# Optimization experiments

Hardware: AMD Instinct MI355X
Metric: run time of the kernel (lower is better)

The kernel has to match this reference:

```python
import jax, jax.numpy as jnp
import numpy as np

MIN_C = 1e-5   # base_c * DYNAMIC_CURVATURE_MIN_RATIO
MAX_C = 10.0   # base_c * DYNAMIC_CURVATURE_MAX_RATIO
T = 0.7
EPS = 1e-7
B, IN_DIM, HID, OUT_DIM = 4096, 4096, 4096, 1024


def _artanh(x):
    x = jnp.clip(x, -1.0 + 1e-5, 1.0 - 1e-5)
    return 0.5 * jnp.log1p(2.0 * x / (1.0 - x))


def _mobius_scalar_mul(r, x, c):
    # r: python float, x: [B,D], c: [B,1] per-row curvature
    sqrt_c = jnp.sqrt(c)
    norm = jnp.clip(jnp.linalg.norm(x, axis=-1, keepdims=True), EPS)
    arg = jnp.clip(sqrt_c * norm, EPS, 1.0 - 1e-5)
    return jnp.tanh(r * _artanh(arg)) * x / (sqrt_c * norm)


def _mobius_add(x, y, c):
    xy = jnp.sum(x * y, axis=-1, keepdims=True)
    x2 = jnp.sum(x * x, axis=-1, keepdims=True)
    y2 = jnp.sum(y * y, axis=-1, keepdims=True)
    num = (1.0 + 2.0 * c * xy + c * y2) * x + (1.0 - c * x2) * y
    den = 1.0 + 2.0 * c * xy + c * c * x2 * y2
    return num / jnp.clip(den, EPS)


def poincare_ball_layer(h, u, c, t):
    # geodesic-style layer: ((1-t) (*) h) (+) (t (*) u) on the Poincare ball
    return _mobius_add(_mobius_scalar_mul(1.0 - t, h, c),
                       _mobius_scalar_mul(t, u, c), c)


def setup_inputs() -> dict:
    key = jax.random.key(0)
    ks = jax.random.split(key, 8)
    std = 0.02  # WEIGHT_INIT_STD_IMPROVED
    return {
        "x": jax.random.normal(ks[0], (B, IN_DIM), jnp.float32),
        "W1": jax.random.normal(ks[1], (IN_DIM, HID), jnp.float32) * std,
        "b1": jnp.zeros((HID,), jnp.float32),
        "W2": jax.random.normal(ks[2], (HID, HID), jnp.float32) * std,
        "b2": jnp.zeros((HID,), jnp.float32),
        "Wout": jax.random.normal(ks[3], (HID, OUT_DIM), jnp.float32) * std,
        "bout": jnp.zeros((OUT_DIM,), jnp.float32),
        "curv_feat": jax.random.normal(ks[4], (16,), jnp.float32) * 0.01,
        "curv_scale": jnp.ones((1,), jnp.float32) * 0.1,
        "proj": jax.random.normal(ks[5], (IN_DIM, 16), jnp.float32),
    }


def reference(x, W1, b1, W2, b2, Wout, bout, curv_feat, curv_scale, proj):
    x_flat = x.reshape(x.shape[0], -1)
    h = jnp.tanh(x_flat @ W1 + b1)            # [B, HID]
    u = jax.nn.sigmoid(h @ W2 + b2)           # [B, HID]
    # adaptive curvature prediction (vectorized over batch)
    x_red = x_flat @ proj                     # [B, 16]
    feat_inter = x_red @ curv_feat            # [B]
    adj = jax.nn.sigmoid(feat_inter + curv_scale[0])
    c = MIN_C + (MAX_C - MIN_C) * adj         # [B]
    c = jnp.clip(c, MIN_C, MAX_C)[:, None]    # [B, 1]
    z = poincare_ball_layer(h, u, c, T)
    # NaN fallback per row (mirrors torch per-sample isnan check)
    z = jnp.where(jnp.any(jnp.isnan(z), axis=1, keepdims=True), h, z)
    return z @ Wout + bout
```

## Files before the change

kernel.cpp:

```cpp
#include <hip/hip_runtime.h>
#include <hip/hip_bf16.h>
#include <math.h>


typedef __attribute__((ext_vector_type(8)))  __bf16 bf16x8;
typedef __attribute__((ext_vector_type(4)))  float  f32x4;
typedef __attribute__((ext_vector_type(8)))  unsigned short us8;

constexpr int BATCH = 4096;
constexpr int IND   = 4096;
constexpr int HIDD  = 4096;
constexpr int OUTD  = 1024;
constexpr float T_C  = 0.7f;
constexpr float MINC = 1e-5f;
constexpr float MAXC = 10.0f;
constexpr float EPSV = 1e-7f;

__device__ __forceinline__ float bf2f(unsigned int us) {
    return __uint_as_float(us << 16);
}
__device__ __forceinline__ unsigned short f2bf(float f) {
    unsigned int u = __float_as_uint(f);
    u = (u + 0x7FFFu + ((u >> 16) & 1u)) >> 16;
    return (unsigned short)u;
}
__device__ __forceinline__ void stage16(const char* src, const unsigned short* dst) {
    __builtin_amdgcn_global_load_lds(
        (const __attribute__((address_space(1))) unsigned int*)src,
        (__attribute__((address_space(3))) unsigned int*)dst, 16, 0, 0);
}

__global__ __launch_bounds__(256)
void cast_curv(const float* __restrict__ x, const float* __restrict__ v,
               const float* __restrict__ cs,
               unsigned short* __restrict__ xb, float* __restrict__ c)
{
    const int row = blockIdx.x;
    const float* xr = x + (size_t)row * IND;
    unsigned short* ob = xb + (size_t)row * IND;
    float s = 0.f;
    for (int i = threadIdx.x; i < IND / 4; i += 256) {
        float4 w  = ((const float4*)xr)[i];
        float4 vv = ((const float4*)v)[i];
        s += w.x * vv.x + w.y * vv.y + w.z * vv.z + w.w * vv.w;
        ushort4 o;
        o.x = f2bf(w.x); o.y = f2bf(w.y); o.z = f2bf(w.z); o.w = f2bf(w.w);
        ((ushort4*)ob)[i] = o;
    }
    #pragma unroll
    for (int o = 32; o > 0; o >>= 1) s += __shfl_down(s, o, 64);
    __shared__ float red[4];
    if ((threadIdx.x & 63) == 0) red[threadIdx.x >> 6] = s;
    __syncthreads();
    if (threadIdx.x == 0) {
        float tot = red[0] + red[1] + red[2] + red[3];
        float adj = 1.0f / (1.0f + expf(-(tot + cs[0])));
        float cc  = MINC + (MAXC - MINC) * adj;
        c[row] = fminf(fmaxf(cc, MINC), MAXC);
    }
}

__global__ __launch_bounds__(256)
void transpose_cast64(const float* __restrict__ in, unsigned short* __restrict__ out,
                      int K, int N)
{
    __shared__ float tile[64][65];
    const int k0 = blockIdx.y * 64;
    const int n0 = blockIdx.x * 64;
    const int t = threadIdx.x;
    #pragma unroll
    for (int i = 0; i < 4; i++) {
        const int idx = i * 256 + t;
        const int r = idx >> 4, c4 = (idx & 15) * 4;
        float4 v = *(const float4*)(&in[(size_t)(k0 + r) * N + n0 + c4]);
        tile[r][c4 + 0] = v.x; tile[r][c4 + 1] = v.y;
        tile[r][c4 + 2] = v.z; tile[r][c4 + 3] = v.w;
    }
    __syncthreads();
    #pragma unroll
    for (int j = 0; j < 2; j++) {
        const int idx = j * 256 + t;
        const int r = idx >> 3, c8 = (idx & 7) * 8;
        us8 o;
        #pragma unroll
        for (int e = 0; e < 8; e++) o[e] = f2bf(tile[c8 + e][r]);
        *(us8*)(&out[(size_t)(n0 + r) * K + k0 + c8]) = o;
    }
}

template<int EPI>
__global__ __launch_bounds__(512, 2)
void gemm256(const unsigned short* __restrict__ A,
             const unsigned short* __restrict__ Bt,
             const float* __restrict__ bias,
             unsigned short* __restrict__ outp,
             int N, int K)
{
    __shared__ unsigned short lds[4 * 256 * 64];

    const int t = threadIdx.x;
    const int w = t >> 6, l = t & 63;
    const int wr = w >> 2, wc = w & 3;
    const int lr = l & 15, lg = l >> 4;

    const int nwg = gridDim.x * gridDim.y;
    const int bid = blockIdx.y * gridDim.x + blockIdx.x;
    const int q8 = nwg >> 3, r8 = nwg & 7;
    const int xcd = bid & 7, off = bid >> 3;
    const int wgid = (xcd < r8 ? xcd * (q8 + 1) : r8 * (q8 + 1) + (xcd - r8) * q8) + off;
    const int by = wgid / gridDim.x;
    const int bx = wgid % gridDim.x;

    const int row0 = by * 256, col0 = bx * 256;
    const unsigned short* Ab = A  + (size_t)row0 * K;
    const unsigned short* Bb = Bt + (size_t)col0 * K;
    const int NT = K >> 6;

    f32x4 acc[8][4] = {};

    const int id0 = t, id1 = 512 + t;
    const int r0 = id0 >> 3, r1 = id1 >> 3;
    const int cb0 = (id0 & 7) * 16, cb1 = (id1 & 7) * 16;
    const int s0 = cb0 ^ ((r0 & 7) << 4), s1 = cb1 ^ ((r1 & 7) << 4);
    const size_t K2 = (size_t)K * 2;
    const char* pA00 = (const char*)Ab + (size_t)r0 * K2 + s0;
    const char* pA01 = (const char*)Ab + (size_t)r1 * K2 + s1;
    const char* pA10 = pA00 + 128 * K2;
    const char* pA11 = pA01 + 128 * K2;
    const char* pB00 = (const char*)Bb + (size_t)r0 * K2 + s0;
    const char* pB01 = (const char*)Bb + (size_t)r1 * K2 + s1;
    const char* pB10 = pB00 + 128 * K2;
    const char* pB11 = pB01 + 128 * K2;
    const int dA0a = id0 * 8,          dA0b = id1 * 8;
    const int dA1a = 8192 + id0 * 8,   dA1b = 8192 + id1 * 8;
    const int dB0a = 32768 + id0 * 8,  dB0b = 32768 + id1 * 8;
    const int dB1a = 40960 + id0 * 8,  dB1b = 40960 + id1 * 8;

    const int sw = (lr & 7) << 4;
    const int c0 = (lg * 16) ^ sw;
    const int c1 = (64 + lg * 16) ^ sw;
    const int aofc0 = (wr * 16 + lr) * 128 + c0;
    const int aofc1 = (wr * 16 + lr) * 128 + c1;
    const int bofc0 = 65536 + (wc * 64 + lr) * 128 + c0;
    const int bofc1 = 65536 + (wc * 64 + lr) * 128 + c1;
    const char* ldsb = (const char*)lds;

    stage16(pA00, lds + dA0a); stage16(pA01, lds + dA0b);
    stage16(pB00, lds + dB0a); stage16(pB01, lds + dB0b);
    stage16(pB10, lds + dB1a); stage16(pB11, lds + dB1b);
    stage16(pA10, lds + dA1a); stage16(pA11, lds + dA1b);
    asm volatile("s_waitcnt vmcnt(0)" ::: "memory");
    __builtin_amdgcn_s_barrier();

    for (int kt = 0; kt < NT; ++kt) {
        const int buf = kt & 1, nb = buf ^ 1;
        const bool pre = (kt + 1 < NT);
        pA00 += 128; pA01 += 128; pA10 += 128; pA11 += 128;
        pB00 += 128; pB01 += 128; pB10 += 128; pB11 += 128;
        const int bufby = buf * 32768;
        const int bsh   = nb * 16384;
        const char* rA0 = ldsb + bufby + aofc0;
        const char* rA1 = ldsb + bufby + aofc1;
        const char* rB0 = ldsb + bufby + bofc0;
        const char* rB1 = ldsb + bufby + bofc1;

        if (pre) {
            stage16(pA00, lds + bsh + dA0a); stage16(pA01, lds + bsh + dA0b);
            stage16(pB00, lds + bsh + dB0a); stage16(pB01, lds + bsh + dB0b);
            stage16(pB10, lds + bsh + dB1a); stage16(pB11, lds + bsh + dB1b);
            stage16(pA10, lds + bsh + dA1a); stage16(pA11, lds + bsh + dA1b);
        }

        bf16x8 bfk[4], afk[4];

        #pragma unroll
        for (int ni = 0; ni < 4; ni++) bfk[ni] = *(const bf16x8*)(rB0 + ni * 2048);
        #pragma unroll
        for (int mi = 0; mi < 4; mi++) afk[mi] = *(const bf16x8*)(rA0 + mi * 4096);
        __builtin_amdgcn_s_setprio(1);
        #pragma unroll
        for (int mi = 0; mi < 4; mi++)
            #pragma unroll
            for (int ni = 0; ni < 4; ni++)
                acc[mi][ni] = __builtin_amdgcn_mfma_f32_16x16x32_bf16(
                    afk[mi], bfk[ni], acc[mi][ni], 0, 0, 0);
        __builtin_amdgcn_s_setprio(0);

        #pragma unroll
        for (int mi = 0; mi < 4; mi++) afk[mi] = *(const bf16x8*)(rA0 + 16384 + mi * 4096);
        __builtin_amdgcn_s_setprio(1);
        #pragma unroll
        for (int mi = 0; mi < 4; mi++)
            #pragma unroll
            for (int ni = 0; ni < 4; ni++)
                acc[4 + mi][ni] = __builtin_amdgcn_mfma_f32_16x16x32_bf16(
                    afk[mi], bfk[ni], acc[4 + mi][ni], 0, 0, 0);
        __builtin_amdgcn_s_setprio(0);

        #pragma unroll
        for (int ni = 0; ni < 4; ni++) bfk[ni] = *(const bf16x8*)(rB1 + ni * 2048);
        #pragma unroll
        for (int mi = 0; mi < 4; mi++) afk[mi] = *(const bf16x8*)(rA1 + mi * 4096);
        __builtin_amdgcn_s_setprio(1);
        #pragma unroll
        for (int mi = 0; mi < 4; mi++)
            #pragma unroll
            for (int ni = 0; ni < 4; ni++)
                acc[mi][ni] = __builtin_amdgcn_mfma_f32_16x16x32_bf16(
                    afk[mi], bfk[ni], acc[mi][ni], 0, 0, 0);
        __builtin_amdgcn_s_setprio(0);

        #pragma unroll
        for (int mi = 0; mi < 4; mi++) afk[mi] = *(const bf16x8*)(rA1 + 16384 + mi * 4096);
        __builtin_amdgcn_s_setprio(1);
        #pragma unroll
        for (int mi = 0; mi < 4; mi++)
            #pragma unroll
            for (int ni = 0; ni < 4; ni++)
                acc[4 + mi][ni] = __builtin_amdgcn_mfma_f32_16x16x32_bf16(
                    afk[mi], bfk[ni], acc[4 + mi][ni], 0, 0, 0);
        __builtin_amdgcn_s_setprio(0);

        asm volatile("s_waitcnt vmcnt(0)" ::: "memory");
        __builtin_amdgcn_s_barrier();
    }

    const int colb = col0 + wc * 64;
    #pragma unroll
    for (int ni = 0; ni < 4; ni++) {
        const int cg = colb + ni * 16 + lr;
        const float bv = bias[cg];
        #pragma unroll
        for (int mi = 0; mi < 8; mi++) {
            #pragma unroll
            for (int r = 0; r < 4; r++) {
                const int rg = row0 + wr * 16 + mi * 32 + lg * 4 + r;
                float v = acc[mi][ni][r] + bv;
                if constexpr (EPI == 0) v = tanhf(v);
                else                    v = 1.0f / (1.0f + expf(-v));
                outp[(size_t)rg * N + cg] = f2bf(v);
            }
        }
    }
}

__global__ __launch_bounds__(512, 2)
void gemm_out128(const unsigned short* __restrict__ A,
                 const unsigned short* __restrict__ Bt,
                 const float* __restrict__ bias,
                 float* __restrict__ outp,
                 int N, int K)
{
    __shared__ unsigned short lds[32768];

    const int t = threadIdx.x;
    const int w = t >> 6, l = t & 63;
    const int wr = w >> 2, wc = w & 3;
    const int lr = l & 15, lg = l >> 4;

    const int nwg = gridDim.x * gridDim.y;
    const int bid = blockIdx.y * gridDim.x + blockIdx.x;
    const int q8 = nwg >> 3, r8 = nwg & 7;
    const int xcd = bid & 7, off = bid >> 3;
    const int wgid = (xcd < r8 ? xcd * (q8 + 1) : r8 * (q8 + 1) + (xcd - r8) * q8) + off;
    const int by = wgid / gridDim.x;
    const int bx = wgid % gridDim.x;

    const int row0 = by * 128, col0 = bx * 128;
    const unsigned short* Ab = A  + (size_t)row0 * K;
    const unsigned short* Bb = Bt + (size_t)col0 * K;
    const int NT = K >> 6;

    f32x4 acc[4][2] = {};

    const int sr = t >> 2;
    const int scb = ((t & 3) * 16) ^ ((sr & 3) << 4);
    const size_t K2 = (size_t)K * 2;
    const char* pAk0 = (const char*)Ab + (size_t)sr * K2 + scb;
    const char* pAk1 = pAk0 + 64;
    const char* pBk0 = (const char*)Bb + (size_t)sr * K2 + scb;
    const char* pBk1 = pBk0 + 64;
    const int dAk0 = t * 8,          dAk1 = 4096 + t * 8;
    const int dBk0 = 16384 + t * 8,  dBk1 = 20480 + t * 8;

    const int csw = (lg * 16) ^ ((lr & 3) << 4);
    const int aof = (wr * 64 + lr) * 64 + csw;
    const int bof = 32768 + (wc * 32 + lr) * 64 + csw;
    const char* ldsb = (const char*)lds;

    stage16(pAk0, lds + dAk0); stage16(pBk0, lds + dBk0);
    stage16(pAk1, lds + dAk1); stage16(pBk1, lds + dBk1);
    asm volatile("s_waitcnt vmcnt(0)" ::: "memory");
    __builtin_amdgcn_s_barrier();

    for (int kt = 0; kt < NT; ++kt) {
        const int buf = kt & 1, nb = buf ^ 1;
        const bool pre = (kt + 1 < NT);
        pAk0 += 128; pAk1 += 128; pBk0 += 128; pBk1 += 128;
        const int bufby = buf * 16384;
        const int bsh   = nb * 8192;
        const char* rA0 = ldsb + bufby + aof;
        const char* rB0 = ldsb + bufby + bof;
        const char* rA1 = rA0 + 8192;
        const char* rB1 = rB0 + 8192;

        if (pre) {
            stage16(pAk0, lds + bsh + dAk0); stage16(pBk0, lds + bsh + dBk0);
            stage16(pAk1, lds + bsh + dAk1); stage16(pBk1, lds + bsh + dBk1);
        }

        bf16x8 af[4], bfr[2];

        #pragma unroll
        for (int nj = 0; nj < 2; nj++) bfr[nj] = *(const bf16x8*)(rB0 + nj * 1024);
        #pragma unroll
        for (int mi = 0; mi < 4; mi++) af[mi] = *(const bf16x8*)(rA0 + mi * 1024);
        __builtin_amdgcn_s_setprio(1);
        #pragma unroll
        for (int mi = 0; mi < 4; mi++)
            #pragma unroll
            for (int nj = 0; nj < 2; nj++)
                acc[mi][nj] = __builtin_amdgcn_mfma_f32_16x16x32_bf16(
                    af[mi], bfr[nj], acc[mi][nj], 0, 0, 0);
        __builtin_amdgcn_s_setprio(0);

        #pragma unroll
        for (int nj = 0; nj < 2; nj++) bfr[nj] = *(const bf16x8*)(rB1 + nj * 1024);
        #pragma unroll
        for (int mi = 0; mi < 4; mi++) af[mi] = *(const bf16x8*)(rA1 + mi * 1024);
        __builtin_amdgcn_s_setprio(1);
        #pragma unroll
        for (int mi = 0; mi < 4; mi++)
            #pragma unroll
            for (int nj = 0; nj < 2; nj++)
                acc[mi][nj] = __builtin_amdgcn_mfma_f32_16x16x32_bf16(
                    af[mi], bfr[nj], acc[mi][nj], 0, 0, 0);
        __builtin_amdgcn_s_setprio(0);

        asm volatile("s_waitcnt vmcnt(0)" ::: "memory");
        __builtin_amdgcn_s_barrier();
    }

    #pragma unroll
    for (int nj = 0; nj < 2; nj++) {
        const int cg = col0 + wc * 32 + nj * 16 + lr;
        const float bv = bias[cg];
        #pragma unroll
        for (int mi = 0; mi < 4; mi++)
            #pragma unroll
            for (int r = 0; r < 4; r++) {
                const int rg = row0 + wr * 64 + mi * 16 + lg * 4 + r;
                outp[(size_t)rg * N + cg] = acc[mi][nj][r] + bv;
            }
    }
}

__global__ __launch_bounds__(256)
void proj_cf(const float* __restrict__ proj, const float* __restrict__ cf,
             float* __restrict__ v)
{
    int i = blockIdx.x * 256 + threadIdx.x;
    if (i < IND) {
        float s = 0.f;
        #pragma unroll
        for (int j = 0; j < 16; j++) s += proj[i * 16 + j] * cf[j];
        v[i] = s;
    }
}

__global__ __launch_bounds__(256)
void poincare_kernel(const unsigned short* __restrict__ hb,
                     const unsigned short* __restrict__ ub,
                     const float* __restrict__ c,
                     unsigned short* __restrict__ zb)
{
    const int row = blockIdx.x;
    const int t = threadIdx.x;
    const size_t base = (size_t)row * HIDD;

    float hv[16], uv[16];
    float h2 = 0.f, u2 = 0.f, hu = 0.f;
    #pragma unroll
    for (int q = 0; q < 2; q++) {
        const int e0 = (q * 256 + t) * 8;
        uint4 hc = *(const uint4*)(hb + base + e0);
        uint4 uc = *(const uint4*)(ub + base + e0);
        const unsigned int hw[4] = {hc.x, hc.y, hc.z, hc.w};
        const unsigned int uw[4] = {uc.x, uc.y, uc.z, uc.w};
        #pragma unroll
        for (int i = 0; i < 4; i++) {
            float h0 = bf2f(hw[i] & 0xFFFFu), h1 = bf2f(hw[i] >> 16);
            float u0 = bf2f(uw[i] & 0xFFFFu), u1 = bf2f(uw[i] >> 16);
            hv[q * 8 + 2 * i]     = h0; hv[q * 8 + 2 * i + 1] = h1;
            uv[q * 8 + 2 * i]     = u0; uv[q * 8 + 2 * i + 1] = u1;
            h2 += h0 * h0 + h1 * h1;
            u2 += u0 * u0 + u1 * u1;
            hu += h0 * u0 + h1 * u1;
        }
    }
    #pragma unroll
    for (int o = 32; o > 0; o >>= 1) {
        h2 += __shfl_down(h2, o, 64);
        u2 += __shfl_down(u2, o, 64);
        hu += __shfl_down(hu, o, 64);
    }
    __shared__ float red[3][4];
    const int w = t >> 6;
    if ((t & 63) == 0) { red[0][w] = h2; red[1][w] = u2; red[2][w] = hu; }
    __syncthreads();
    h2 = red[0][0] + red[0][1] + red[0][2] + red[0][3];
    u2 = red[1][0] + red[1][1] + red[1][2] + red[1][3];
    hu = red[2][0] + red[2][1] + red[2][2] + red[2][3];

    const float cc = c[row];
    const float sc = sqrtf(cc);
    float nh = fmaxf(sqrtf(h2), EPSV);
    float nu = fmaxf(sqrtf(u2), EPSV);
    float ah = fminf(fmaxf(sc * nh, EPSV), 1.0f - 1e-5f);
    float au = fminf(fmaxf(sc * nu, EPSV), 1.0f - 1e-5f);
    float ath = 0.5f * log1pf(2.0f * ah / (1.0f - ah));
    float atu = 0.5f * log1pf(2.0f * au / (1.0f - au));
    float alpha = tanhf((1.0f - T_C) * ath) / (sc * nh);
    float beta  = tanhf(T_C * atu) / (sc * nu);
    float x2 = alpha * alpha * h2;
    float y2 = beta * beta * u2;
    float xy = alpha * beta * hu;
    float den = 1.0f + 2.0f * cc * xy + cc * cc * x2 * y2;
    den = fmaxf(den, EPSV);
    float ca = (1.0f + 2.0f * cc * xy + cc * y2) * alpha / den;
    float cb = (1.0f - cc * x2) * beta / den;
    if (isnan(ca) || isnan(cb)) { ca = 1.0f; cb = 0.0f; }

    #pragma unroll
    for (int q = 0; q < 2; q++) {
        const int e0 = (q * 256 + t) * 8;
        unsigned int ow[4];
        #pragma unroll
        for (int i = 0; i < 4; i++) {
            float z0 = ca * hv[q * 8 + 2 * i]     + cb * uv[q * 8 + 2 * i];
            float z1 = ca * hv[q * 8 + 2 * i + 1] + cb * uv[q * 8 + 2 * i + 1];
            ow[i] = (unsigned int)f2bf(z0) | ((unsigned int)f2bf(z1) << 16);
        }
        *(uint4*)(zb + base + e0) = make_uint4(ow[0], ow[1], ow[2], ow[3]);
    }
}

extern "C" void kernel_launch(void* const* d_in, const int* in_sizes, int n_in,
                              void* d_out, int out_size, void* d_ws, size_t ws_size,
                              hipStream_t stream)
{
    const float* x    = (const float*)d_in[0];
    const float* W1   = (const float*)d_in[1];
    const float* b1   = (const float*)d_in[2];
    const float* W2   = (const float*)d_in[3];
    const float* b2   = (const float*)d_in[4];
    const float* Wout = (const float*)d_in[5];
    const float* bout = (const float*)d_in[6];
    const float* cf   = (const float*)d_in[7];
    const float* cs   = (const float*)d_in[8];
    const float* proj = (const float*)d_in[9];
    float* out = (float*)d_out;

    char* ws = (char*)d_ws;
    unsigned short* x_bf = (unsigned short*)(ws);
    unsigned short* w_bf = (unsigned short*)(ws + (33554432));
    unsigned short* h_bf = (unsigned short*)(ws + (67108864));
    unsigned short* u_bf = (unsigned short*)(ws + (100663296));
    float* vvec = (float*)(ws + 134217728);
    float* cvec = (float*)(ws + 134217728 + 16384);

    proj_cf<<<IND / 256, 256, 0, stream>>>(proj, cf, vvec);
    cast_curv<<<BATCH, 256, 0, stream>>>(x, vvec, cs, x_bf, cvec);

    transpose_cast64<<<dim3(HIDD / 64, IND / 64), 256, 0, stream>>>(W1, w_bf, IND, HIDD);
    gemm256<0><<<dim3(HIDD / 256, BATCH / 256), 512, 0, stream>>>(x_bf, w_bf, b1, h_bf, HIDD, IND);

    transpose_cast64<<<dim3(HIDD / 64, HIDD / 64), 256, 0, stream>>>(W2, w_bf, HIDD, HIDD);
    gemm256<1><<<dim3(HIDD / 256, BATCH / 256), 512, 0, stream>>>(h_bf, w_bf, b2, u_bf, HIDD, HIDD);

    poincare_kernel<<<BATCH, 256, 0, stream>>>(h_bf, u_bf, cvec, x_bf);

    transpose_cast64<<<dim3(OUTD / 64, HIDD / 64), 256, 0, stream>>>(Wout, w_bf, HIDD, OUTD);
    gemm_out128<<<dim3(OUTD / 128, BATCH / 128), 512, 0, stream>>>(x_bf, w_bf, bout, out, OUTD, HIDD);
}
```

Baseline: 387.6 us.

## Restructure 256x256 GEMM main loop into fine-grained staged pipeline

Reorganizes the LDS layout of the 256-tile GEMM so A and B live in separate half-buffers, and B is prefetched two K-steps ahead while A is prefetched one step ahead. Each K-step is split into four phases, each interleaving small A-fragment LDS reads, one piece of global-to-LDS staging, barriers and 16 MFMAs. The goal is to spread memory traffic across the MFMA work and avoid the large end-of-iteration vmcnt(0) stall. Warp row mapping changes to contiguous 128-row halves. In exchange it adds many more barriers per iteration and depends on fragile vmcnt accounting.

```diff
diff --git a/kernel.cpp b/kernel.cpp
--- a/kernel.cpp
+++ b/kernel.cpp
@@ -96,7 +96,7 @@
              unsigned short* __restrict__ outp,
              int N, int K)
 {
-    __shared__ unsigned short lds[4 * 256 * 64];
+    __shared__ unsigned short lds[65536];
 
     const int t = threadIdx.x;
     const int w = t >> 6, l = t & 63;
@@ -120,8 +120,8 @@
 
     const int id0 = t, id1 = 512 + t;
     const int r0 = id0 >> 3, r1 = id1 >> 3;
-    const int cb0 = (id0 & 7) * 16, cb1 = (id1 & 7) * 16;
-    const int s0 = cb0 ^ ((r0 & 7) << 4), s1 = cb1 ^ ((r1 & 7) << 4);
+    const int s0 = ((id0 & 7) * 16) ^ ((r0 & 7) << 4);
+    const int s1 = ((id1 & 7) * 16) ^ ((r1 & 7) << 4);
     const size_t K2 = (size_t)K * 2;
     const char* pA00 = (const char*)Ab + (size_t)r0 * K2 + s0;
     const char* pA01 = (const char*)Ab + (size_t)r1 * K2 + s1;
@@ -133,96 +133,104 @@
     const char* pB11 = pB01 + 128 * K2;
     const int dA0a = id0 * 8,          dA0b = id1 * 8;
     const int dA1a = 8192 + id0 * 8,   dA1b = 8192 + id1 * 8;
-    const int dB0a = 32768 + id0 * 8,  dB0b = 32768 + id1 * 8;
-    const int dB1a = 40960 + id0 * 8,  dB1b = 40960 + id1 * 8;
+    const int dB0a = 16384 + id0 * 8,  dB0b = 16384 + id1 * 8;
+    const int dB1a = 24576 + id0 * 8,  dB1b = 24576 + id1 * 8;
 
     const int sw = (lr & 7) << 4;
     const int c0 = (lg * 16) ^ sw;
     const int c1 = (64 + lg * 16) ^ sw;
-    const int aofc0 = (wr * 16 + lr) * 128 + c0;
-    const int aofc1 = (wr * 16 + lr) * 128 + c1;
-    const int bofc0 = 65536 + (wc * 64 + lr) * 128 + c0;
-    const int bofc1 = 65536 + (wc * 64 + lr) * 128 + c1;
+    const int aof = (wr * 128 + lr) * 128;
+    const int bof = 32768 + (wc * 64 + lr) * 128;
     const char* ldsb = (const char*)lds;
 
     stage16(pA00, lds + dA0a); stage16(pA01, lds + dA0b);
+    stage16(pA10, lds + dA1a); stage16(pA11, lds + dA1b);
     stage16(pB00, lds + dB0a); stage16(pB01, lds + dB0b);
     stage16(pB10, lds + dB1a); stage16(pB11, lds + dB1b);
-    stage16(pA10, lds + dA1a); stage16(pA11, lds + dA1b);
-    asm volatile("s_waitcnt vmcnt(0)" ::: "memory");
+    stage16(pB00 + 128, lds + 32768 + dB0a); stage16(pB01 + 128, lds + 32768 + dB0b);
+    stage16(pB10 + 128, lds + 32768 + dB1a); stage16(pB11 + 128, lds + 32768 + dB1b);
+    asm volatile("s_waitcnt vmcnt(4)" ::: "memory");
     __builtin_amdgcn_s_barrier();
+    pB00 += 128; pB01 += 128; pB10 += 128; pB11 += 128;
 
     for (int kt = 0; kt < NT; ++kt) {
         const int buf = kt & 1, nb = buf ^ 1;
-        const bool pre = (kt + 1 < NT);
         pA00 += 128; pA01 += 128; pA10 += 128; pA11 += 128;
         pB00 += 128; pB01 += 128; pB10 += 128; pB11 += 128;
-        const int bufby = buf * 32768;
-        const int bsh   = nb * 16384;
-        const char* rA0 = ldsb + bufby + aofc0;
-        const char* rA1 = ldsb + bufby + aofc1;
-        const char* rB0 = ldsb + bufby + bofc0;
-        const char* rB1 = ldsb + bufby + bofc1;
-
-        if (pre) {
-            stage16(pA00, lds + bsh + dA0a); stage16(pA01, lds + bsh + dA0b);
-            stage16(pB00, lds + bsh + dB0a); stage16(pB01, lds + bsh + dB0b);
-            stage16(pB10, lds + bsh + dB1a); stage16(pB11, lds + bsh + dB1b);
-            stage16(pA10, lds + bsh + dA1a); stage16(pA11, lds + bsh + dA1b);
-        }
-
-        bf16x8 bfk[4], afk[4];
-
-        #pragma unroll
-        for (int ni = 0; ni < 4; ni++) bfk[ni] = *(const bf16x8*)(rB0 + ni * 2048);
-        #pragma unroll
-        for (int mi = 0; mi < 4; mi++) afk[mi] = *(const bf16x8*)(rA0 + mi * 4096);
+        const bool preA = (kt + 1 < NT);
+        const bool preB = (kt + 2 < NT);
+        const char* rA = ldsb + buf * 65536 + aof;
+        const char* rB = ldsb + buf * 65536 + bof;
+        unsigned short* sbA = lds + nb * 32768;
+        unsigned short* sbB = lds + buf * 32768;
+
+        bf16x8 bB[4][2], aF[2][2];
+
+        #pragma unroll
+        for (int ni = 0; ni < 4; ni++) {
+            bB[ni][0] = *(const bf16x8*)(rB + ni * 2048 + c0);
+            bB[ni][1] = *(const bf16x8*)(rB + ni * 2048 + c1);
+        }
+        aF[0][0] = *(const bf16x8*)(rA + 0 * 2048 + c0);
+        aF[0][1] = *(const bf16x8*)(rA + 0 * 2048 + c1);
+        aF[1][0] = *(const bf16x8*)(rA + 1 * 2048 + c0);
+        aF[1][1] = *(const bf16x8*)(rA + 1 * 2048 + c1);
+        if (preA) { stage16(pA00, sbA + dA0a); stage16(pA01, sbA + dA0b); }
+        __builtin_amdgcn_sched_barrier(0);
+        __builtin_amdgcn_s_barrier();
+        asm volatile("s_waitcnt lgkmcnt(0)" ::: "memory");
+        __builtin_amdgcn_sched_barrier(0);
         __builtin_amdgcn_s_setprio(1);
         #pragma unroll
-        for (int mi = 0; mi < 4; mi++)
+        for (int s = 0; s < 2; s++)
             #pragma unroll
             for (int ni = 0; ni < 4; ni++)
-                acc[mi][ni] = __builtin_amdgcn_mfma_f32_16x16x32_bf16(
-                    afk[mi], bfk[ni], acc[mi][ni], 0, 0, 0);
+                acc[s][ni] = __builtin_amdgcn_mfma_f32_16x16x32_bf16(
+                    aF[s][0], bB[ni][0], acc[s][ni], 0, 0, 0);
+        #pragma unroll
+        for (int s = 0; s < 2; s++)
+            #pragma unroll
+            for (int ni = 0; ni < 4; ni++)
+                acc[s][ni] = __builtin_amdgcn_mfma_f32_16x16x32_bf16(
+                    aF[s][1], bB[ni][1], acc[s][ni], 0, 0, 0);
         __builtin_amdgcn_s_setprio(0);
-
-        #pragma unroll
-        for (int mi = 0; mi < 4; mi++) afk[mi] = *(const bf16x8*)(rA0 + 16384 + mi * 4096);
-        __builtin_amdgcn_s_setprio(1);
-        #pragma unroll
-        for (int mi = 0; mi < 4; mi++)
-            #pragma unroll
-            for (int ni = 0; ni < 4; ni++)
-                acc[4 + mi][ni] = __builtin_amdgcn_mfma_f32_16x16x32_bf16(
-                    afk[mi], bfk[ni], acc[4 + mi][ni], 0, 0, 0);
-        __builtin_amdgcn_s_setprio(0);
-
-        #pragma unroll
-        for (int ni = 0; ni < 4; ni++) bfk[ni] = *(const bf16x8*)(rB1 + ni * 2048);
-        #pragma unroll
-        for (int mi = 0; mi < 4; mi++) afk[mi] = *(const bf16x8*)(rA1 + mi * 4096);
-        __builtin_amdgcn_s_setprio(1);
-        #pragma unroll
-        for (int mi = 0; mi < 4; mi++)
-            #pragma unroll
-            for (int ni = 0; ni < 4; ni++)
-                acc[mi][ni] = __builtin_amdgcn_mfma_f32_16x16x32_bf16(
-                    afk[mi], bfk[ni], acc[mi][ni], 0, 0, 0);
-        __builtin_amdgcn_s_setprio(0);
-
-        #pragma unroll
-        for (int mi = 0; mi < 4; mi++) afk[mi] = *(const bf16x8*)(rA1 + 16384 + mi * 4096);
-        __builtin_amdgcn_s_setprio(1);
-        #pragma unroll
-        for (int mi = 0; mi < 4; mi++)
-            #pragma unroll
-            for (int ni = 0; ni < 4; ni++)
-                acc[4 + mi][ni] = __builtin_amdgcn_mfma_f32_16x16x32_bf16(
-                    afk[mi], bfk[ni], acc[4 + mi][ni], 0, 0, 0);
-        __builtin_amdgcn_s_setprio(0);
-
-        asm volatile("s_waitcnt vmcnt(0)" ::: "memory");
+        __builtin_amdgcn_sched_barrier(0);
         __builtin_amdgcn_s_barrier();
+
+        #pragma unroll
+        for (int p = 1; p < 4; p++) {
+            aF[0][0] = *(const bf16x8*)(rA + (2 * p) * 2048 + c0);
+            aF[0][1] = *(const bf16x8*)(rA + (2 * p) * 2048 + c1);
+            aF[1][0] = *(const bf16x8*)(rA + (2 * p + 1) * 2048 + c0);
+            aF[1][1] = *(const bf16x8*)(rA + (2 * p + 1) * 2048 + c1);
+            if (p == 1 && preA) { stage16(pA10, sbA + dA1a); stage16(pA11, sbA + dA1b); }
+            if (p == 2 && preB) { stage16(pB00, sbB + dB0a); stage16(pB01, sbB + dB0b); }
+            if (p == 3 && preB) { stage16(pB10, sbB + dB1a); stage16(pB11, sbB + dB1b); }
+            __builtin_amdgcn_sched_barrier(0);
+            __builtin_amdgcn_s_barrier();
+            asm volatile("s_waitcnt lgkmcnt(0)" ::: "memory");
+            __builtin_amdgcn_sched_barrier(0);
+            __builtin_amdgcn_s_setprio(1);
+            #pragma unroll
+            for (int s = 0; s < 2; s++)
+                #pragma unroll
+                for (int ni = 0; ni < 4; ni++)
+                    acc[2 * p + s][ni] = __builtin_amdgcn_mfma_f32_16x16x32_bf16(
+                        aF[s][0], bB[ni][0], acc[2 * p + s][ni], 0, 0, 0);
+            #pragma unroll
+            for (int s = 0; s < 2; s++)
+                #pragma unroll
+                for (int ni = 0; ni < 4; ni++)
+                    acc[2 * p + s][ni] = __builtin_amdgcn_mfma_f32_16x16x32_bf16(
+                        aF[s][1], bB[ni][1], acc[2 * p + s][ni], 0, 0, 0);
+            __builtin_amdgcn_s_setprio(0);
+            __builtin_amdgcn_sched_barrier(0);
+            if (p == 3) {
+                if (preB) asm volatile("s_waitcnt vmcnt(4)" ::: "memory");
+                else      asm volatile("s_waitcnt vmcnt(0)" ::: "memory");
+            }
+            __builtin_amdgcn_s_barrier();
+        }
     }
 
     const int colb = col0 + wc * 64;
@@ -234,7 +242,7 @@
         for (int mi = 0; mi < 8; mi++) {
             #pragma unroll
             for (int r = 0; r < 4; r++) {
-                const int rg = row0 + wr * 16 + mi * 32 + lg * 4 + r;
+                const int rg = row0 + wr * 128 + mi * 16 + lg * 4 + r;
                 float v = acc[mi][ni][r] + bv;
                 if constexpr (EPI == 0) v = tanhf(v);
                 else                    v = 1.0f / (1.0f + expf(-v));
```

Result: slower. 398.9 us (+2.9%).
